# Kernel tuning notes

Hardware: AMD Instinct MI355X
Metric: run time of the kernel (lower is better)

Reference implementation:

```python
import jax, jax.numpy as jnp
import numpy as np

GAMMA = 0.9
TOL = 1e-06
MAX_ITER = 50


def solve_fp(A, b, gamma, act, max_iter, tol):
    """Find fixed point of x = act(gamma * A @ x + b), matching the torch loop
    (break *before* accepting x_next when ||x - x_next|| < tol)."""
    def cond(carry):
        x, itr, done = carry
        return (itr < max_iter) & (~done)

    def body(carry):
        x, itr, done = carry
        x_next = act(gamma * jnp.matmul(A, x) + b)  # [H, N, 1]
        conv = jnp.linalg.norm(x - x_next) < tol
        x_new = jnp.where(conv, x, x_next)          # keep old x on break
        itr_new = itr + jnp.where(conv, 0, 1)
        return (x_new, itr_new, conv)

    x0 = jnp.zeros_like(b)
    x, _, _ = jax.lax.while_loop(cond, body, (x0, jnp.int32(0), jnp.bool_(False)))
    return x


def setup_inputs() -> dict:
    key = jax.random.key(0)
    kA, kb = jax.random.split(key)
    H, N = 8, 2048
    # scale so spectral radius of GAMMA*A < 1 (circular law: radius ~ sqrt(N)*std)
    A = jax.random.normal(kA, (H, N, N), dtype=jnp.float32) * (0.4 / np.sqrt(N))
    b = jax.random.normal(kb, (H, N, 1), dtype=jnp.float32)
    return {"A": A, "b": b}


def reference(A, b):
    act = jnp.tanh  # activation="Tanh"
    z_star = solve_fp(A, b, GAMMA, act, MAX_ITER, TOL)        # no-grad fixed point
    z = act(GAMMA * jnp.matmul(A, z_star) + b)                # one differentiable step
    return z[..., 0]                                          # squeeze -> [H, N]
```

## Files before the change

kernel.cpp:

```cpp
#include <hip/hip_runtime.h>
#include <hip/hip_bf16.h>


#define FPL_GAMMA 0.9f
#define INT8_STEPS 10
#define FB_STEPS 15
#define COOP_H 8
#define COOP_N 2048
#define COOP_HN (COOP_H * COOP_N)
#define MAX_HN 65536
#define SWZ4(i) ((i) ^ (((i) >> 3) & 7))

__device__ float g_x[2][MAX_HN];
__device__ int   g_is_f32;
__device__ unsigned int g_flag[COOP_H * 32];

__device__ __forceinline__ float bf2f(unsigned short u) {
    union { unsigned int i; float f; } v; v.i = ((unsigned int)u) << 16; return v.f;
}

__device__ __forceinline__ float4 ld_f4_cp(const void* p) {
    float4 r;
    asm volatile("global_load_dwordx4 %0, %1, off sc0 sc1\n\ts_waitcnt vmcnt(0)"
                 : "=v"(r) : "v"(p) : "memory");
    return r;
}
__device__ __forceinline__ unsigned int ld_u32_cp(const void* p) {
    unsigned int r;
    asm volatile("global_load_dword %0, %1, off sc0 sc1\n\ts_waitcnt vmcnt(0)"
                 : "=v"(r) : "v"(p) : "memory");
    return r;
}
__device__ __forceinline__ void st_u32_cp(void* p, unsigned int v) {
    asm volatile("global_store_dword %0, %1, off sc0 sc1"
                 :: "v"(p), "v"(v) : "memory");
}

__global__ __launch_bounds__(256) void fpl_probe(const unsigned short* __restrict__ A) {
    const int t = threadIdx.x;
    g_flag[t] = 0u;
    if (t < 64) {
        int bad = 0;
#pragma unroll
        for (int k = 0; k < 4; ++k) {
            const float av = fabsf(bf2f(A[(t << 2) + k]));
            if (!(av <= 1e3f)) bad = 1;
        }
        const unsigned long long any = __ballot(bad);
        if (t == 0) g_is_f32 = (any != 0ull) ? 1 : 0;
    }
}

__global__ __launch_bounds__(256) void fpl_init(const void* __restrict__ bv, int hn) {
    int i = blockIdx.x * 256 + threadIdx.x;
    if (i < hn) {
        float bval = g_is_f32 ? ((const float*)bv)[i]
                              : bf2f(((const unsigned short*)bv)[i]);
        g_x[0][i] = tanhf(bval);
    }
}

__device__ __forceinline__ float dec4(unsigned int w, const float4 x, float acc) {
    acc = fmaf((float)((int)(w << 24) >> 24), x.x, acc);
    acc = fmaf((float)((int)(w << 16) >> 24), x.y, acc);
    acc = fmaf((float)((int)(w <<  8) >> 24), x.z, acc);
    acc = fmaf((float)((int)w >> 24),         x.w, acc);
    return acc;
}

__device__ __forceinline__ void quant_row(const float4* v4, int lrow, int lane,
                                          unsigned int* aq, float* rowscale) {
    float m = 0.f;
#pragma unroll
    for (int k = 0; k < 8; ++k)
        m = fmaxf(m, fmaxf(fmaxf(fabsf(v4[k].x), fabsf(v4[k].y)),
                           fmaxf(fabsf(v4[k].z), fabsf(v4[k].w))));
#pragma unroll
    for (int off = 32; off > 0; off >>= 1)
        m = fmaxf(m, __shfl_xor(m, off, 64));
    m = fmaxf(m, 1e-30f);
    const float inv = 127.0f / m;
    if (lane == 0) rowscale[lrow] = m * (1.0f / 127.0f);
    unsigned int* aqr = aq + lrow * 512;
#pragma unroll
    for (int k = 0; k < 8; ++k) {
        const int q0 = (int)rintf(v4[k].x * inv);
        const int q1 = (int)rintf(v4[k].y * inv);
        const int q2 = (int)rintf(v4[k].z * inv);
        const int q3 = (int)rintf(v4[k].w * inv);
        aqr[(k << 6) + lane] = (unsigned int)(q0 & 255)
                             | ((unsigned int)(q1 & 255) << 8)
                             | ((unsigned int)(q2 & 255) << 16)
                             | ((unsigned int)(q3 & 255) << 24);
    }
}

__global__ __launch_bounds__(512)
void fpl_coop(const void* __restrict__ Av,
              const void* __restrict__ bv,
              float* __restrict__ out) {
    __shared__ unsigned int aq[64 * 512];
    __shared__ float xs[COOP_N];
    __shared__ float red[64 * 65];
    __shared__ float rowscale[64];

    const int tid  = threadIdx.x;
    const int wave = tid >> 6;
    const int lane = tid & 63;
    const int bid  = blockIdx.x;
    const int head = bid & 7;
    const int jblk = bid >> 3;
    const int rowBase = jblk << 6;
    const bool isf32 = (g_is_f32 != 0);
    const int lrow0 = wave << 3;

    if (isf32) {
        const float* Ab = (const float*)Av;
        const size_t grow0 = (size_t)(head * COOP_N + rowBase + lrow0);
        float4 cur[8], nxt[8];
        {
            const float* Ar = Ab + (grow0 << 11);
#pragma unroll
            for (int k = 0; k < 8; ++k)
                cur[k] = *(const float4*)(Ar + ((k << 8) + (lane << 2)));
        }
#pragma unroll 1
        for (int r = 0; r < 8; ++r) {
            if (r < 7) {
                const float* Ar = Ab + ((grow0 + r + 1) << 11);
#pragma unroll
                for (int k = 0; k < 8; ++k)
                    nxt[k] = *(const float4*)(Ar + ((k << 8) + (lane << 2)));
            }
            quant_row(cur, lrow0 + r, lane, aq, rowscale);
#pragma unroll
            for (int k = 0; k < 8; ++k) cur[k] = nxt[k];
        }
    } else {
#pragma unroll 1
        for (int r = 0; r < 8; ++r) {
            const int lrow = lrow0 + r;
            const size_t grow = (size_t)(head * COOP_N + rowBase + lrow);
            const unsigned short* Ar = (const unsigned short*)Av + (grow << 11);
            float4 v4[8];
#pragma unroll
            for (int k = 0; k < 8; ++k) {
                const ushort4 t = *(const ushort4*)(Ar + ((k << 8) + (lane << 2)));
                v4[k] = make_float4(bf2f(t.x), bf2f(t.y), bf2f(t.z), bf2f(t.w));
            }
            quant_row(v4, lrow, lane, aq, rowscale);
        }
    }

    {
        float4 bb;
        if (isf32) bb = ((const float4*)bv)[(head << 9) + tid];
        else {
            const ushort4 t = ((const ushort4*)bv)[(head << 9) + tid];
            bb = make_float4(bf2f(t.x), bf2f(t.y), bf2f(t.z), bf2f(t.w));
        }
        ((float4*)xs)[SWZ4(tid)] =
            make_float4(tanhf(bb.x), tanhf(bb.y), tanhf(bb.z), tanhf(bb.w));
    }

    const int rl   = tid >> 3;
    const int gRow = head * COOP_N + rowBase + rl;
    float breg = 0.f;
    if ((tid & 7) == 0)
        breg = isf32 ? ((const float*)bv)[gRow]
                     : bf2f(((const unsigned short*)bv)[gRow]);

    __syncthreads();
    const float sreg = rowscale[rl];
    const float4* xsf4 = (const float4*)xs;

    for (int s = 0; s < INT8_STEPS; ++s) {
        float acc[8];
#pragma unroll
        for (int r = 0; r < 8; ++r) acc[r] = 0.f;
#pragma unroll
        for (int j = 0; j < 2; ++j) {
            const int base = (j << 8) + (lane << 2);
            const float4 x0 = xsf4[SWZ4(base + 0)];
            const float4 x1 = xsf4[SWZ4(base + 1)];
            const float4 x2 = xsf4[SWZ4(base + 2)];
            const float4 x3 = xsf4[SWZ4(base + 3)];
#pragma unroll
            for (int r = 0; r < 8; ++r) {
                const uint4 w = *(const uint4*)(aq + (lrow0 + r) * 512 + base);
                float a = acc[r];
                a = dec4(w.x, x0, a);
                a = dec4(w.y, x1, a);
                a = dec4(w.z, x2, a);
                a = dec4(w.w, x3, a);
                acc[r] = a;
            }
        }

#pragma unroll
        for (int r = 0; r < 8; ++r)
            red[(lrow0 + r) * 65 + lane] = acc[r];
        __syncthreads();

        const int c = tid & 7;
        const float* rr = &red[rl * 65 + (c << 3)];
        float v = ((rr[0] + rr[1]) + (rr[2] + rr[3]))
                + ((rr[4] + rr[5]) + (rr[6] + rr[7]));
        v += __shfl_xor(v, 1, 64);
        v += __shfl_xor(v, 2, 64);
        v += __shfl_xor(v, 4, 64);

        if (c == 0)
            st_u32_cp(&g_x[s & 1][gRow],
                      __float_as_uint(tanhf(FPL_GAMMA * sreg * v + breg)));

        __syncthreads();
        if (tid == 0)
            st_u32_cp(&g_flag[(head << 5) + jblk], (unsigned int)(s + 1));

        {
            const unsigned int tgt = (unsigned int)(s + 1);
            const unsigned int* fp = &g_flag[(head << 5) + (tid & 31)];
            for (;;) {
                const unsigned int f = ld_u32_cp(fp);
                if (__all((int)(f >= tgt))) break;
                __builtin_amdgcn_s_sleep(1);
            }
        }

        {
            const float4 xv = ld_f4_cp((const float4*)&g_x[s & 1][head << 11] + tid);
            ((float4*)xs)[SWZ4(tid)] = xv;
        }
        __syncthreads();
    }

#pragma unroll 1
    for (int r = 0; r < 8; ++r) {
        const int lrow = lrow0 + r;
        const size_t grow = (size_t)(head * COOP_N + rowBase + lrow);
        float acc = 0.f;
        if (isf32) {
            const float* Ar = (const float*)Av + (grow << 11);
#pragma unroll
            for (int k = 0; k < 8; ++k) {
                const float4 a = *(const float4*)(Ar + ((k << 8) + (lane << 2)));
                const float4 x = xsf4[SWZ4((k << 6) + lane)];
                acc += a.x * x.x + a.y * x.y + a.z * x.z + a.w * x.w;
            }
        } else {
            const unsigned short* Ar = (const unsigned short*)Av + (grow << 11);
#pragma unroll
            for (int k = 0; k < 8; ++k) {
                const ushort4 t = *(const ushort4*)(Ar + ((k << 8) + (lane << 2)));
                const float4 x = xsf4[SWZ4((k << 6) + lane)];
                acc += bf2f(t.x) * x.x + bf2f(t.y) * x.y
                     + bf2f(t.z) * x.z + bf2f(t.w) * x.w;
            }
        }
#pragma unroll
        for (int off = 32; off > 0; off >>= 1)
            acc += __shfl_xor(acc, off, 64);
        if (lane == 0) {
            const float bval = isf32 ? ((const float*)bv)[grow]
                                     : bf2f(((const unsigned short*)bv)[grow]);
            out[grow] = tanhf(FPL_GAMMA * acc + bval);
        }
    }
}

template <bool FINAL>
__global__ __launch_bounds__(256) void fpl_step_raw(const void* __restrict__ Av,
                                                    const void* __restrict__ bv,
                                                    int src, int N,
                                                    float* __restrict__ out) {
    extern __shared__ float xsd[];
    const int rowBlocks = N >> 4;
    const int head = blockIdx.x / rowBlocks;
    const int r0   = (blockIdx.x % rowBlocks) << 4;
    const int tid  = threadIdx.x;
    const float4* xg = (const float4*)(g_x[src] + head * N);
    for (int j = tid; j < (N >> 2); j += 256) ((float4*)xsd)[j] = xg[j];
    __syncthreads();
    const int wave = tid >> 6, lane = tid & 63;
    const int row = r0 + (wave << 2);
    float acc0 = 0.f, acc1 = 0.f, acc2 = 0.f, acc3 = 0.f;
    const bool isf32 = (g_is_f32 != 0);
    if (isf32) {
        const float* A0 = (const float*)Av + (size_t)(head * N + row) * N;
        for (int cb = 0; cb < N; cb += 256) {
            const int c = cb + (lane << 2);
            const float4 xv = *(const float4*)(xsd + c);
            const float4 a0 = *(const float4*)(A0 + c);
            const float4 a1 = *(const float4*)(A0 + N + c);
            const float4 a2 = *(const float4*)(A0 + 2 * N + c);
            const float4 a3 = *(const float4*)(A0 + 3 * N + c);
            acc0 += a0.x*xv.x + a0.y*xv.y + a0.z*xv.z + a0.w*xv.w;
            acc1 += a1.x*xv.x + a1.y*xv.y + a1.z*xv.z + a1.w*xv.w;
            acc2 += a2.x*xv.x + a2.y*xv.y + a2.z*xv.z + a2.w*xv.w;
            acc3 += a3.x*xv.x + a3.y*xv.y + a3.z*xv.z + a3.w*xv.w;
        }
    } else {
        const unsigned short* A0 = (const unsigned short*)Av + (size_t)(head * N + row) * N;
        for (int cb = 0; cb < N; cb += 256) {
            const int c = cb + (lane << 2);
            const float4 xv = *(const float4*)(xsd + c);
            const ushort4 a0 = *(const ushort4*)(A0 + c);
            const ushort4 a1 = *(const ushort4*)(A0 + N + c);
            const ushort4 a2 = *(const ushort4*)(A0 + 2 * N + c);
            const ushort4 a3 = *(const ushort4*)(A0 + 3 * N + c);
            acc0 += bf2f(a0.x)*xv.x + bf2f(a0.y)*xv.y + bf2f(a0.z)*xv.z + bf2f(a0.w)*xv.w;
            acc1 += bf2f(a1.x)*xv.x + bf2f(a1.y)*xv.y + bf2f(a1.z)*xv.z + bf2f(a1.w)*xv.w;
            acc2 += bf2f(a2.x)*xv.x + bf2f(a2.y)*xv.y + bf2f(a2.z)*xv.z + bf2f(a2.w)*xv.w;
            acc3 += bf2f(a3.x)*xv.x + bf2f(a3.y)*xv.y + bf2f(a3.z)*xv.z + bf2f(a3.w)*xv.w;
        }
    }
#pragma unroll
    for (int off = 32; off > 0; off >>= 1) {
        acc0 += __shfl_xor(acc0, off, 64);
        acc1 += __shfl_xor(acc1, off, 64);
        acc2 += __shfl_xor(acc2, off, 64);
        acc3 += __shfl_xor(acc3, off, 64);
    }
    if (lane < 4) {
        float acc = (lane == 0) ? acc0 : (lane == 1) ? acc1 : (lane == 2) ? acc2 : acc3;
        const int idx = head * N + row + lane;
        const float bval = isf32 ? ((const float*)bv)[idx]
                                 : bf2f(((const unsigned short*)bv)[idx]);
        const float y = tanhf(FPL_GAMMA * acc + bval);
        if (FINAL) out[idx] = y;
        else       g_x[1 - src][idx] = y;
    }
}

extern "C" void kernel_launch(void* const* d_in, const int* in_sizes, int n_in,
                              void* d_out, int out_size, void* d_ws, size_t ws_size,
                              hipStream_t stream) {
    (void)d_ws; (void)ws_size; (void)n_in; (void)out_size;
    const void* A = d_in[0];
    const void* b = d_in[1];
    long szA = in_sizes[0], szb = in_sizes[1];
    if (szA < szb) { const void* t = A; A = b; b = t; long s = szA; szA = szb; szb = s; }
    const int HN = (int)szb;
    const int N  = (int)(szA / szb);
    float* out = (float*)d_out;

    fpl_probe<<<dim3(1), dim3(256), 0, stream>>>((const unsigned short*)A);

    bool done = false;
    if (N == COOP_N && HN == COOP_HN) {
        void* args[] = { (void*)&A, (void*)&b, (void*)&out };
        hipError_t rc = hipLaunchCooperativeKernel((const void*)fpl_coop,
                                                   dim3(256), dim3(512),
                                                   args, 0, stream);
        done = (rc == hipSuccess);
    }
    if (!done) {
        fpl_init<<<dim3((HN + 255) / 256), dim3(256), 0, stream>>>(b, HN);
        const int grid = HN >> 4;
        const size_t lds = (size_t)N * sizeof(float);
        int src = 0;
        for (int s = 0; s < FB_STEPS; ++s) {
            fpl_step_raw<false><<<dim3(grid), dim3(256), lds, stream>>>(A, b, src, N, nullptr);
            src ^= 1;
        }
        fpl_step_raw<true><<<dim3(grid), dim3(256), lds, stream>>>(A, b, src, N, out);
    }
}
```

Measured before the change: 272.4 us.

## Use agent-scope cache bits for inter-block sync when trial handshake succeeds

Adds a startup handshake in which each head's blocks exchange an epoch token using loads and stores with only sc0 (no sc1). If every block sees all tokens, the run switches to these cheaper cache-policy loads and stores for the per-step flag and x exchange; otherwise it keeps the sc0 sc1 system-coherent path. Flags are tagged with an epoch so stale values from earlier launches are ignored, and polling loops are now capped. The aim is lower latency in the ten per-step grid barriers, at the cost of a startup handshake, extra vmcnt waits, and dependence on the trial correctly showing that the weaker coherence is enough.

```diff
diff --git a/kernel.cpp b/kernel.cpp
--- a/kernel.cpp
+++ b/kernel.cpp
@@ -10,35 +10,49 @@
 #define COOP_HN (COOP_H * COOP_N)
 #define MAX_HN 65536
 #define SWZ4(i) ((i) ^ (((i) >> 3) & 7))
+#define TRIAL_BOUND 1024
+#define POLL_CAP (1u << 22)
 
 __device__ float g_x[2][MAX_HN];
 __device__ int   g_is_f32;
 __device__ unsigned int g_flag[COOP_H * 32];
+__device__ unsigned int g_tok[COOP_H * 32];
+__device__ unsigned int g_v[COOP_H * 32];
+__device__ unsigned int g_epoch;
 
 __device__ __forceinline__ float bf2f(unsigned short u) {
     union { unsigned int i; float f; } v; v.i = ((unsigned int)u) << 16; return v.f;
 }
 
-__device__ __forceinline__ float4 ld_f4_cp(const void* p) {
+__device__ __forceinline__ void st_ex32(bool fast, void* p, unsigned int v) {
+    if (fast) asm volatile("global_store_dword %0, %1, off sc0"
+                           :: "v"(p), "v"(v) : "memory");
+    else      asm volatile("global_store_dword %0, %1, off sc0 sc1"
+                           :: "v"(p), "v"(v) : "memory");
+}
+__device__ __forceinline__ unsigned int ld_ex32(bool fast, const void* p) {
+    unsigned int r;
+    if (fast) asm volatile("global_load_dword %0, %1, off sc0\n\ts_waitcnt vmcnt(0)"
+                           : "=v"(r) : "v"(p) : "memory");
+    else      asm volatile("global_load_dword %0, %1, off sc0 sc1\n\ts_waitcnt vmcnt(0)"
+                           : "=v"(r) : "v"(p) : "memory");
+    return r;
+}
+__device__ __forceinline__ float4 ld_ex128(bool fast, const void* p) {
     float4 r;
-    asm volatile("global_load_dwordx4 %0, %1, off sc0 sc1\n\ts_waitcnt vmcnt(0)"
-                 : "=v"(r) : "v"(p) : "memory");
+    if (fast) asm volatile("global_load_dwordx4 %0, %1, off sc0\n\ts_waitcnt vmcnt(0)"
+                           : "=v"(r) : "v"(p) : "memory");
+    else      asm volatile("global_load_dwordx4 %0, %1, off sc0 sc1\n\ts_waitcnt vmcnt(0)"
+                           : "=v"(r) : "v"(p) : "memory");
     return r;
-}
-__device__ __forceinline__ unsigned int ld_u32_cp(const void* p) {
-    unsigned int r;
-    asm volatile("global_load_dword %0, %1, off sc0 sc1\n\ts_waitcnt vmcnt(0)"
-                 : "=v"(r) : "v"(p) : "memory");
-    return r;
-}
-__device__ __forceinline__ void st_u32_cp(void* p, unsigned int v) {
-    asm volatile("global_store_dword %0, %1, off sc0 sc1"
-                 :: "v"(p), "v"(v) : "memory");
 }
 
 __global__ __launch_bounds__(256) void fpl_probe(const unsigned short* __restrict__ A) {
     const int t = threadIdx.x;
     g_flag[t] = 0u;
+    g_tok[t]  = 0u;
+    g_v[t]    = 0u;
+    if (t == 0) g_epoch = g_epoch + 1u;
     if (t < 64) {
         int bad = 0;
 #pragma unroll
@@ -170,9 +184,37 @@
         breg = isf32 ? ((const float*)bv)[gRow]
                      : bf2f(((const unsigned short*)bv)[gRow]);
 
+    const unsigned int epoch = ld_ex32(false, &g_epoch);
+
+    bool fast;
+    {
+        if (tid == 0) st_ex32(true, &g_tok[(head << 5) + jblk], epoch);
+        asm volatile("s_waitcnt vmcnt(0)" ::: "memory");
+        bool ok = false;
+        const unsigned int* tp = &g_tok[(head << 5) + (lane & 31)];
+        for (int it = 0; it < TRIAL_BOUND; ++it) {
+            const unsigned int v = ld_ex32(true, tp);
+            if (__all((int)(v == epoch))) { ok = true; break; }
+            __builtin_amdgcn_s_sleep(1);
+        }
+        if (tid == 0)
+            st_ex32(false, &g_v[(head << 5) + jblk],
+                    (epoch << 1) | (ok ? 1u : 0u));
+        asm volatile("s_waitcnt vmcnt(0)" ::: "memory");
+        const unsigned int* vp = &g_v[(head << 5) + (lane & 31)];
+        unsigned int w = 0u;
+        for (unsigned int it = 0; it < POLL_CAP; ++it) {
+            w = ld_ex32(false, vp);
+            if (__all((int)((w >> 1) == epoch))) break;
+            __builtin_amdgcn_s_sleep(1);
+        }
+        fast = __all((int)(w == ((epoch << 1) | 1u)));
+    }
+
     __syncthreads();
     const float sreg = rowscale[rl];
     const float4* xsf4 = (const float4*)xs;
+    const unsigned int ftag = epoch << 4;
 
     for (int s = 0; s < INT8_STEPS; ++s) {
         float acc[8];
@@ -211,25 +253,28 @@
         v += __shfl_xor(v, 4, 64);
 
         if (c == 0)
-            st_u32_cp(&g_x[s & 1][gRow],
-                      __float_as_uint(tanhf(FPL_GAMMA * sreg * v + breg)));
+            st_ex32(fast, &g_x[s & 1][gRow],
+                    __float_as_uint(tanhf(FPL_GAMMA * sreg * v + breg)));
+        asm volatile("s_waitcnt vmcnt(0)" ::: "memory");
 
         __syncthreads();
         if (tid == 0)
-            st_u32_cp(&g_flag[(head << 5) + jblk], (unsigned int)(s + 1));
+            st_ex32(fast, &g_flag[(head << 5) + jblk],
+                    ftag + (unsigned int)(s + 1));
 
         {
-            const unsigned int tgt = (unsigned int)(s + 1);
+            const unsigned int tgt = ftag + (unsigned int)(s + 1);
             const unsigned int* fp = &g_flag[(head << 5) + (tid & 31)];
-            for (;;) {
-                const unsigned int f = ld_u32_cp(fp);
+            for (unsigned int it = 0; it < POLL_CAP; ++it) {
+                const unsigned int f = ld_ex32(fast, fp);
                 if (__all((int)(f >= tgt))) break;
                 __builtin_amdgcn_s_sleep(1);
             }
         }
 
         {
-            const float4 xv = ld_f4_cp((const float4*)&g_x[s & 1][head << 11] + tid);
+            const float4 xv = ld_ex128(fast,
+                                       (const float4*)&g_x[s & 1][head << 11] + tid);
             ((float4*)xs)[SWZ4(tid)] = xv;
         }
         __syncthreads();
```

Result: slower. 395.1 us (+45.1%).

## Relax inter-block barrier into asynchronous single-buffer iteration with more int8 steps

Applied to the files above, without the earlier changes.

Blocks now share one x buffer. Each block publishes its rows, then optimistically reads the whole x vector. It only waits if peer flags show blocks more than one step behind, which turns the strict grid-wide barrier per step into a bounded-staleness asynchronous (chaotic) fixed-point iteration. To make up for the mixed-age iterates, the int8 step count rises from 10 to 13, and spin waits get a poll cap. The goal is to cut the barrier wait time per iteration, at the cost of extra matvec steps, nondeterministic intermediate values, and possible races that the later fp32 refinement has to absorb.

```diff
diff --git a/kernel.cpp b/kernel.cpp
--- a/kernel.cpp
+++ b/kernel.cpp
@@ -3,13 +3,14 @@
 
 
 #define FPL_GAMMA 0.9f
-#define INT8_STEPS 10
+#define INT8_STEPS 13
 #define FB_STEPS 15
 #define COOP_H 8
 #define COOP_N 2048
 #define COOP_HN (COOP_H * COOP_N)
 #define MAX_HN 65536
 #define SWZ4(i) ((i) ^ (((i) >> 3) & 7))
+#define POLL_CAP (1u << 22)
 
 __device__ float g_x[2][MAX_HN];
 __device__ int   g_is_f32;
@@ -19,21 +20,21 @@
     union { unsigned int i; float f; } v; v.i = ((unsigned int)u) << 16; return v.f;
 }
 
-__device__ __forceinline__ float4 ld_f4_cp(const void* p) {
+__device__ __forceinline__ void st_cp32(void* p, unsigned int v) {
+    asm volatile("global_store_dword %0, %1, off sc0 sc1"
+                 :: "v"(p), "v"(v) : "memory");
+}
+__device__ __forceinline__ unsigned int ld_cp32(const void* p) {
+    unsigned int r;
+    asm volatile("global_load_dword %0, %1, off sc0 sc1\n\ts_waitcnt vmcnt(0)"
+                 : "=v"(r) : "v"(p) : "memory");
+    return r;
+}
+__device__ __forceinline__ float4 ld_cp128(const void* p) {
     float4 r;
     asm volatile("global_load_dwordx4 %0, %1, off sc0 sc1\n\ts_waitcnt vmcnt(0)"
                  : "=v"(r) : "v"(p) : "memory");
     return r;
-}
-__device__ __forceinline__ unsigned int ld_u32_cp(const void* p) {
-    unsigned int r;
-    asm volatile("global_load_dword %0, %1, off sc0 sc1\n\ts_waitcnt vmcnt(0)"
-                 : "=v"(r) : "v"(p) : "memory");
-    return r;
-}
-__device__ __forceinline__ void st_u32_cp(void* p, unsigned int v) {
-    asm volatile("global_store_dword %0, %1, off sc0 sc1"
-                 :: "v"(p), "v"(v) : "memory");
 }
 
 __global__ __launch_bounds__(256) void fpl_probe(const unsigned short* __restrict__ A) {
@@ -170,11 +171,37 @@
         breg = isf32 ? ((const float*)bv)[gRow]
                      : bf2f(((const unsigned short*)bv)[gRow]);
 
+    if ((tid & 7) == 0)
+        st_cp32(&g_x[0][gRow], __float_as_uint(tanhf(breg)));
+    asm volatile("s_waitcnt vmcnt(0)" ::: "memory");
+
     __syncthreads();
     const float sreg = rowscale[rl];
     const float4* xsf4 = (const float4*)xs;
-
-    for (int s = 0; s < INT8_STEPS; ++s) {
+    const int c = tid & 7;
+
+    if (tid == 0) st_cp32(&g_flag[(head << 5) + jblk], 1u);
+
+    unsigned int* const fbase = &g_flag[(head << 5)];
+    const float4* const gx4   = (const float4*)&g_x[0][head << 11];
+
+    for (int i = 1; i <= INT8_STEPS; ++i) {
+        if (i >= 2) {
+            float4 xv = ld_cp128(gx4 + tid);
+            unsigned int f = ld_cp32(fbase + (tid & 31));
+            if (!__all((int)(f >= (unsigned int)i))) {
+                const unsigned int tgt = (unsigned int)(i - 1);
+                for (unsigned int it = 0; it < POLL_CAP; ++it) {
+                    f = ld_cp32(fbase + (tid & 31));
+                    if (__all((int)(f >= tgt))) break;
+                    __builtin_amdgcn_s_sleep(1);
+                }
+                xv = ld_cp128(gx4 + tid);
+            }
+            ((float4*)xs)[SWZ4(tid)] = xv;
+            __syncthreads();
+        }
+
         float acc[8];
 #pragma unroll
         for (int r = 0; r < 8; ++r) acc[r] = 0.f;
@@ -202,7 +229,6 @@
             red[(lrow0 + r) * 65 + lane] = acc[r];
         __syncthreads();
 
-        const int c = tid & 7;
         const float* rr = &red[rl * 65 + (c << 3)];
         float v = ((rr[0] + rr[1]) + (rr[2] + rr[3]))
                 + ((rr[4] + rr[5]) + (rr[6] + rr[7]));
@@ -211,27 +237,23 @@
         v += __shfl_xor(v, 4, 64);
 
         if (c == 0)
-            st_u32_cp(&g_x[s & 1][gRow],
-                      __float_as_uint(tanhf(FPL_GAMMA * sreg * v + breg)));
-
+            st_cp32(&g_x[0][gRow],
+                    __float_as_uint(tanhf(FPL_GAMMA * sreg * v + breg)));
+        asm volatile("s_waitcnt vmcnt(0)" ::: "memory");
         __syncthreads();
         if (tid == 0)
-            st_u32_cp(&g_flag[(head << 5) + jblk], (unsigned int)(s + 1));
-
-        {
-            const unsigned int tgt = (unsigned int)(s + 1);
-            const unsigned int* fp = &g_flag[(head << 5) + (tid & 31)];
-            for (;;) {
-                const unsigned int f = ld_u32_cp(fp);
-                if (__all((int)(f >= tgt))) break;
-                __builtin_amdgcn_s_sleep(1);
-            }
-        }
-
-        {
-            const float4 xv = ld_f4_cp((const float4*)&g_x[s & 1][head << 11] + tid);
-            ((float4*)xs)[SWZ4(tid)] = xv;
-        }
+            st_cp32(fbase + jblk, (unsigned int)(i + 1));
+    }
+
+    {
+        const unsigned int tgt = (unsigned int)(INT8_STEPS + 1);
+        for (unsigned int it = 0; it < POLL_CAP; ++it) {
+            const unsigned int f = ld_cp32(fbase + (tid & 31));
+            if (__all((int)(f >= tgt))) break;
+            __builtin_amdgcn_s_sleep(1);
+        }
+        const float4 xv = ld_cp128(gx4 + tid);
+        ((float4*)xs)[SWZ4(tid)] = xv;
         __syncthreads();
     }
 
```

After: 295.9 us. +8.6%, slower.

## Replace per-block flag barrier with epoch-tagged value words for inter-block exchange

Applied to the files above, without the earlier changes.

Each row's new x value is now stored together with an epoch/step tag in a single 64-bit word. Consumers poll the tagged data directly instead of waiting on a separate per-block flag array and then reloading x. This drops one __syncthreads, the flag store and a separate data load per step, fusing the synchronisation with the data fetch. It also raises the int8 step count from 10 to 13, which adds compute, and bounds the poll loop with a cap, which risks using stale values on timeout.

```diff
diff --git a/kernel.cpp b/kernel.cpp
--- a/kernel.cpp
+++ b/kernel.cpp
@@ -3,42 +3,46 @@
 
 
 #define FPL_GAMMA 0.9f
-#define INT8_STEPS 10
+#define INT8_STEPS 13
 #define FB_STEPS 15
 #define COOP_H 8
 #define COOP_N 2048
 #define COOP_HN (COOP_H * COOP_N)
 #define MAX_HN 65536
 #define SWZ4(i) ((i) ^ (((i) >> 3) & 7))
+#define POLL_CAP (1u << 22)
 
 __device__ float g_x[2][MAX_HN];
+__device__ __align__(16) uint2 g_xt[MAX_HN];
 __device__ int   g_is_f32;
-__device__ unsigned int g_flag[COOP_H * 32];
+__device__ unsigned int g_epoch;
 
 __device__ __forceinline__ float bf2f(unsigned short u) {
     union { unsigned int i; float f; } v; v.i = ((unsigned int)u) << 16; return v.f;
 }
 
-__device__ __forceinline__ float4 ld_f4_cp(const void* p) {
-    float4 r;
-    asm volatile("global_load_dwordx4 %0, %1, off sc0 sc1\n\ts_waitcnt vmcnt(0)"
-                 : "=v"(r) : "v"(p) : "memory");
-    return r;
-}
-__device__ __forceinline__ unsigned int ld_u32_cp(const void* p) {
+__device__ __forceinline__ unsigned int ld_cp32(const void* p) {
     unsigned int r;
     asm volatile("global_load_dword %0, %1, off sc0 sc1\n\ts_waitcnt vmcnt(0)"
                  : "=v"(r) : "v"(p) : "memory");
     return r;
 }
-__device__ __forceinline__ void st_u32_cp(void* p, unsigned int v) {
-    asm volatile("global_store_dword %0, %1, off sc0 sc1"
+__device__ __forceinline__ void st_cp64(void* p, uint2 v) {
+    asm volatile("global_store_dwordx2 %0, %1, off sc0 sc1"
                  :: "v"(p), "v"(v) : "memory");
+}
+__device__ __forceinline__ void ld2_cp128(const void* p, uint4& a, uint4& b) {
+    asm volatile("global_load_dwordx4 %0, %2, off sc0 sc1\n\t"
+                 "global_load_dwordx4 %1, %3, off sc0 sc1\n\t"
+                 "s_waitcnt vmcnt(0)"
+                 : "=&v"(a), "=&v"(b)
+                 : "v"(p), "v"((const void*)((const char*)p + 16))
+                 : "memory");
 }
 
 __global__ __launch_bounds__(256) void fpl_probe(const unsigned short* __restrict__ A) {
     const int t = threadIdx.x;
-    g_flag[t] = 0u;
+    if (t == 0) g_epoch = g_epoch + 1u;
     if (t < 64) {
         int bad = 0;
 #pragma unroll
@@ -103,6 +107,7 @@
     __shared__ float xs[COOP_N];
     __shared__ float red[64 * 65];
     __shared__ float rowscale[64];
+    __shared__ unsigned int sh_base;
 
     const int tid  = threadIdx.x;
     const int wave = tid >> 6;
@@ -114,6 +119,8 @@
     const bool isf32 = (g_is_f32 != 0);
     const int lrow0 = wave << 3;
 
+    if (tid == 0) sh_base = ld_cp32(&g_epoch) << 6;
+
     if (isf32) {
         const float* Ab = (const float*)Av;
         const size_t grow0 = (size_t)(head * COOP_N + rowBase + lrow0);
@@ -171,23 +178,30 @@
                      : bf2f(((const unsigned short*)bv)[gRow]);
 
     __syncthreads();
+    const unsigned int base = sh_base;
     const float sreg = rowscale[rl];
     const float4* xsf4 = (const float4*)xs;
-
-    for (int s = 0; s < INT8_STEPS; ++s) {
+    const int c = tid & 7;
+
+    if (c == 0)
+        st_cp64(&g_xt[gRow], make_uint2(__float_as_uint(tanhf(breg)), base + 1u));
+
+    const uint4* const gx4 = (const uint4*)&g_xt[head << 11];
+
+    for (int i = 1; i <= INT8_STEPS; ++i) {
         float acc[8];
 #pragma unroll
         for (int r = 0; r < 8; ++r) acc[r] = 0.f;
 #pragma unroll
         for (int j = 0; j < 2; ++j) {
-            const int base = (j << 8) + (lane << 2);
-            const float4 x0 = xsf4[SWZ4(base + 0)];
-            const float4 x1 = xsf4[SWZ4(base + 1)];
-            const float4 x2 = xsf4[SWZ4(base + 2)];
-            const float4 x3 = xsf4[SWZ4(base + 3)];
+            const int bb = (j << 8) + (lane << 2);
+            const float4 x0 = xsf4[SWZ4(bb + 0)];
+            const float4 x1 = xsf4[SWZ4(bb + 1)];
+            const float4 x2 = xsf4[SWZ4(bb + 2)];
+            const float4 x3 = xsf4[SWZ4(bb + 3)];
 #pragma unroll
             for (int r = 0; r < 8; ++r) {
-                const uint4 w = *(const uint4*)(aq + (lrow0 + r) * 512 + base);
+                const uint4 w = *(const uint4*)(aq + (lrow0 + r) * 512 + bb);
                 float a = acc[r];
                 a = dec4(w.x, x0, a);
                 a = dec4(w.y, x1, a);
@@ -202,7 +216,6 @@
             red[(lrow0 + r) * 65 + lane] = acc[r];
         __syncthreads();
 
-        const int c = tid & 7;
         const float* rr = &red[rl * 65 + (c << 3)];
         float v = ((rr[0] + rr[1]) + (rr[2] + rr[3]))
                 + ((rr[4] + rr[5]) + (rr[6] + rr[7]));
@@ -211,27 +224,40 @@
         v += __shfl_xor(v, 4, 64);
 
         if (c == 0)
-            st_u32_cp(&g_x[s & 1][gRow],
-                      __float_as_uint(tanhf(FPL_GAMMA * sreg * v + breg)));
-
-        __syncthreads();
-        if (tid == 0)
-            st_u32_cp(&g_flag[(head << 5) + jblk], (unsigned int)(s + 1));
-
-        {
-            const unsigned int tgt = (unsigned int)(s + 1);
-            const unsigned int* fp = &g_flag[(head << 5) + (tid & 31)];
-            for (;;) {
-                const unsigned int f = ld_u32_cp(fp);
-                if (__all((int)(f >= tgt))) break;
+            st_cp64(&g_xt[gRow],
+                    make_uint2(__float_as_uint(tanhf(FPL_GAMMA * sreg * v + breg)),
+                               base + (unsigned int)(i + 1)));
+
+        if (i < INT8_STEPS) {
+            const unsigned int need = base + (unsigned int)i;
+            uint4 a, b;
+            for (unsigned int it = 0; it < POLL_CAP; ++it) {
+                ld2_cp128(gx4 + (tid << 1), a, b);
+                const int ok = (a.y >= need) & (a.w >= need)
+                             & (b.y >= need) & (b.w >= need);
+                if (__all(ok)) break;
                 __builtin_amdgcn_s_sleep(1);
             }
-        }
-
-        {
-            const float4 xv = ld_f4_cp((const float4*)&g_x[s & 1][head << 11] + tid);
-            ((float4*)xs)[SWZ4(tid)] = xv;
-        }
+            ((float4*)xs)[SWZ4(tid)] =
+                make_float4(__uint_as_float(a.x), __uint_as_float(a.z),
+                            __uint_as_float(b.x), __uint_as_float(b.z));
+            __syncthreads();
+        }
+    }
+
+    {
+        const unsigned int need = base + (unsigned int)(INT8_STEPS + 1);
+        uint4 a, b;
+        for (unsigned int it = 0; it < POLL_CAP; ++it) {
+            ld2_cp128(gx4 + (tid << 1), a, b);
+            const int ok = (a.y >= need) & (a.w >= need)
+                         & (b.y >= need) & (b.w >= need);
+            if (__all(ok)) break;
+            __builtin_amdgcn_s_sleep(1);
+        }
+        ((float4*)xs)[SWZ4(tid)] =
+            make_float4(__uint_as_float(a.x), __uint_as_float(a.z),
+                        __uint_as_float(b.x), __uint_as_float(b.z));
         __syncthreads();
     }
 
```

Result: slower. 298.7 us (+9.7%).
